# Kernel optimization log

Measured on AMD Instinct MI355X. Metric: run time of the kernel, lower is better.

Reference implementation:

```python
import jax, jax.numpy as jnp
import numpy as np

KSIZE = 51  # radius=50 is even -> incremented to 51 in __init__


def _gaussian_1d(ksize):
    # cv2.getGaussianKernel with sigma<=0: sigma = 0.3*((ksize-1)*0.5 - 1) + 0.8
    sigma = 0.3 * ((ksize - 1) * 0.5 - 1) + 0.8
    x = np.arange(ksize, dtype=np.float64) - (ksize - 1) / 2
    g = np.exp(-(x * x) / (2.0 * sigma * sigma))
    g = g / g.sum()
    return g.astype(np.float32)


def _blur(img, kernel1d):
    """Separable Gaussian blur with reflect padding.
    Mathematically identical to the 2D conv with outer(g, g) in the torch code.
    img: (b, c, h, w), kernel1d: (k,)
    """
    k = kernel1d.shape[0]
    p = k // 2
    b, c, h, w = img.shape
    x = jnp.pad(img, ((0, 0), (0, 0), (p, p), (p, p)), mode='reflect')
    x = x.reshape(b * c, 1, h + 2 * p, w + 2 * p)
    # vertical pass then horizontal pass (conv vs correlation irrelevant: symmetric kernel)
    kv = kernel1d.reshape(1, 1, k, 1)
    kh = kernel1d.reshape(1, 1, 1, k)
    dn = ('NCHW', 'OIHW', 'NCHW')
    x = jax.lax.conv_general_dilated(x, kv, (1, 1), 'VALID', dimension_numbers=dn)
    x = jax.lax.conv_general_dilated(x, kh, (1, 1), 'VALID', dimension_numbers=dn)
    return x.reshape(b, c, h, w)


def setup_inputs() -> dict:
    key = jax.random.key(0)
    img = jax.random.uniform(key, (16, 3, 512, 512), dtype=jnp.float32)
    kernel1d = jnp.asarray(_gaussian_1d(KSIZE))
    return {"img": img, "kernel1d": kernel1d}


def reference(img, kernel1d):
    weight = 0.5
    threshold = 10.0
    blur = _blur(img, kernel1d)
    residual = img - blur
    mask = (jnp.abs(residual) * 255.0 > threshold).astype(img.dtype)
    soft_mask = _blur(mask, kernel1d)
    sharp = jnp.clip(img + weight * residual, 0.0, 1.0)
    return soft_mask * sharp + (1.0 - soft_mask) * img
```

## Files before the change

### kernel.cpp

```cpp
#include <hip/hip_runtime.h>
#include <hip/hip_bf16.h>


constexpr int IMG = 512;
constexpr int NIMG = 48;
constexpr int K = 51, P = 25;
constexpr int CB = 64;
constexpr int RB = 128;
constexpr int WAVES = 8;
constexpr int VB = 16;
constexpr int NLOOP = VB + K - 1;
constexpr int TR = RB + 2 * P;
constexpr int TRS = RB + 1;
constexpr int LDS_FLOATS = TR * CB;

__device__ __forceinline__ float bf2f(unsigned short u) {
    unsigned int x = (unsigned int)u << 16;
    return __builtin_bit_cast(float, x);
}
__device__ __forceinline__ unsigned short f2bf(float f) {
    unsigned int u = __builtin_bit_cast(unsigned int, f);
    u += 0x7FFF + ((u >> 16) & 1);
    return (unsigned short)(u >> 16);
}

template <int SRCB, int LOADM, int STOREM>
__global__ __launch_bounds__(512) void pass_kern(const void* __restrict__ srcv,
                                                 const float* __restrict__ img,
                                                 const unsigned short* __restrict__ res,
                                                 void* __restrict__ dstv,
                                                 const float* __restrict__ k1d) {
    __shared__ float lds[LDS_FLOATS];
    const int lane = threadIdx.x & 63;
    const int wvu = __builtin_amdgcn_readfirstlane(threadIdx.x >> 6);
    const int c0 = blockIdx.x * CB;
    const int r0 = blockIdx.y * RB;
    const size_t base = (size_t)blockIdx.z * (IMG * IMG);

    for (int r = wvu; r < TR; r += WAVES) {
        int y = r0 - P + r;
        const int ya = y < 0 ? -y : y;
        y = min(ya, 2 * IMG - 2 - y);
        const size_t si = base + (size_t)y * IMG + c0 + lane;
        float v = SRCB ? bf2f(((const unsigned short*)srcv)[si])
                       : ((const float*)srcv)[si];
        if (LOADM == 1) v = (fabsf(v) * 255.0f > 10.0f) ? 1.0f : 0.0f;
        lds[r * CB + lane] = v;
    }

    float kern[K];
#pragma unroll
    for (int k = 0; k < K; ++k) kern[k] = k1d[k];

    __syncthreads();

    float acc[VB];
#pragma unroll
    for (int o = 0; o < VB; ++o) acc[o] = 0.f;

    const int trow0 = wvu * VB;
#pragma unroll
    for (int r = 0; r < NLOOP; ++r) {
        const float v = lds[(trow0 + r) * CB + lane];
#pragma unroll
        for (int o = 0; o < VB; ++o) {
            const int k = r - o;
            if (0 <= k && k < K) acc[o] = fmaf(kern[k], v, acc[o]);
        }
    }

    __syncthreads();

#pragma unroll
    for (int o = 0; o < VB; ++o) lds[lane * TRS + trow0 + o] = acc[o];
    __syncthreads();

#pragma unroll
    for (int i = 0; i < 8; ++i) {
        const int cc = wvu * 8 + i;
#pragma unroll
        for (int j = 0; j < 2; ++j) {
            const int rr = j * 64 + lane;
            const float bv = lds[cc * TRS + rr];
            const size_t di = base + (size_t)(c0 + cc) * IMG + (r0 + rr);
            if (STOREM == 0) {
                ((unsigned short*)dstv)[di] = f2bf(bv);
            } else if (STOREM == 1) {
                ((unsigned short*)dstv)[di] = f2bf(img[di] - bv);
            } else {
                const float iv = img[di];
                const float rv = bf2f(res[di]);
                float sharp = fmaf(0.5f, rv, iv);
                sharp = fminf(fmaxf(sharp, 0.f), 1.f);
                ((float*)dstv)[di] = fmaf(bv, sharp - iv, iv);
            }
        }
    }
}

extern "C" void kernel_launch(void* const* d_in, const int* in_sizes, int n_in,
                              void* d_out, int out_size, void* d_ws, size_t ws_size,
                              hipStream_t stream) {
    (void)in_sizes; (void)n_in; (void)out_size; (void)ws_size;
    const float* img = (const float*)d_in[0];
    const float* k1d = (const float*)d_in[1];
    float* out = (float*)d_out;
    unsigned short* vb = (unsigned short*)d_ws;
    unsigned short* rs = (unsigned short*)d_ws + (size_t)NIMG * IMG * IMG;

    const dim3 grid(IMG / CB, IMG / RB, NIMG);

    pass_kern<0, 0, 0><<<grid, 512, 0, stream>>>(img, nullptr, nullptr, vb, k1d);
    pass_kern<1, 0, 1><<<grid, 512, 0, stream>>>(vb, img, nullptr, rs, k1d);
    pass_kern<1, 1, 0><<<grid, 512, 0, stream>>>(rs, nullptr, nullptr, vb, k1d);
    pass_kern<1, 0, 2><<<grid, 512, 0, stream>>>(vb, img, rs, out, k1d);
}
```

Baseline: 100.9 us.

## Stage column tiles in LDS as swizzled bf16 and read four rows per load

The LDS staging buffer now holds bf16 values in a column-major, XOR-swizzled layout, so each lane reads four consecutive rows with a single 8-byte LDS load instead of one float per row. This cuts the number of LDS read instructions in the vertical convolution loop and shrinks the staging footprint. In exchange, the first pass now rounds the fp32 input to bf16 before convolving, which adds precision loss. Bit extraction and conversion instructions are also added to the inner loop.

```diff
diff --git a/kernel.cpp b/kernel.cpp
--- a/kernel.cpp
+++ b/kernel.cpp
@@ -10,9 +10,11 @@
 constexpr int WAVES = 8;
 constexpr int VB = 16;
 constexpr int NLOOP = VB + K - 1;
+constexpr int NCHUNK = 17;
 constexpr int TR = RB + 2 * P;
+constexpr int SROW = 256;
 constexpr int TRS = RB + 1;
-constexpr int LDS_FLOATS = TR * CB;
+constexpr int LDS_BYTES = CB * TRS * 4;
 
 __device__ __forceinline__ float bf2f(unsigned short u) {
     unsigned int x = (unsigned int)u << 16;
@@ -24,13 +26,20 @@
     return (unsigned short)(u >> 16);
 }
 
+__device__ __forceinline__ int sidx(int c, int r) {
+    return c * SROW + (r ^ ((c & 15) << 2));
+}
+
 template <int SRCB, int LOADM, int STOREM>
 __global__ __launch_bounds__(512) void pass_kern(const void* __restrict__ srcv,
                                                  const float* __restrict__ img,
                                                  const unsigned short* __restrict__ res,
                                                  void* __restrict__ dstv,
                                                  const float* __restrict__ k1d) {
-    __shared__ float lds[LDS_FLOATS];
+    __shared__ unsigned char ldsraw[LDS_BYTES];
+    unsigned short* st = (unsigned short*)ldsraw;
+    float* tr = (float*)ldsraw;
+
     const int lane = threadIdx.x & 63;
     const int wvu = __builtin_amdgcn_readfirstlane(threadIdx.x >> 6);
     const int c0 = blockIdx.x * CB;
@@ -42,10 +51,17 @@
         const int ya = y < 0 ? -y : y;
         y = min(ya, 2 * IMG - 2 - y);
         const size_t si = base + (size_t)y * IMG + c0 + lane;
-        float v = SRCB ? bf2f(((const unsigned short*)srcv)[si])
-                       : ((const float*)srcv)[si];
-        if (LOADM == 1) v = (fabsf(v) * 255.0f > 10.0f) ? 1.0f : 0.0f;
-        lds[r * CB + lane] = v;
+        unsigned short u;
+        if (SRCB) {
+            u = ((const unsigned short*)srcv)[si];
+            if (LOADM == 1) {
+                const float v = bf2f(u);
+                u = (fabsf(v) * 255.0f > 10.0f) ? 0x3F80 : 0;
+            }
+        } else {
+            u = f2bf(((const float*)srcv)[si]);
+        }
+        st[sidx(lane, r)] = u;
     }
 
     float kern[K];
@@ -59,20 +75,35 @@
     for (int o = 0; o < VB; ++o) acc[o] = 0.f;
 
     const int trow0 = wvu * VB;
+    const int sbase = lane * SROW;
+    const int sx = (lane & 15) << 2;
 #pragma unroll
-    for (int r = 0; r < NLOOP; ++r) {
-        const float v = lds[(trow0 + r) * CB + lane];
+    for (int t = 0; t < NCHUNK; ++t) {
+        const int rb4 = trow0 + 4 * t;
+        const uint2 ch = *(const uint2*)(&st[sbase + (rb4 ^ sx)]);
 #pragma unroll
-        for (int o = 0; o < VB; ++o) {
-            const int k = r - o;
-            if (0 <= k && k < K) acc[o] = fmaf(kern[k], v, acc[o]);
+        for (int i = 0; i < 4; ++i) {
+            const int r = 4 * t + i;
+            if (r < NLOOP) {
+                const unsigned short uu =
+                    (i == 0) ? (unsigned short)ch.x :
+                    (i == 1) ? (unsigned short)(ch.x >> 16) :
+                    (i == 2) ? (unsigned short)ch.y :
+                               (unsigned short)(ch.y >> 16);
+                const float v = bf2f(uu);
+#pragma unroll
+                for (int o = 0; o < VB; ++o) {
+                    const int k = r - o;
+                    if (0 <= k && k < K) acc[o] = fmaf(kern[k], v, acc[o]);
+                }
+            }
         }
     }
 
     __syncthreads();
 
 #pragma unroll
-    for (int o = 0; o < VB; ++o) lds[lane * TRS + trow0 + o] = acc[o];
+    for (int o = 0; o < VB; ++o) tr[lane * TRS + trow0 + o] = acc[o];
     __syncthreads();
 
 #pragma unroll
@@ -81,7 +112,7 @@
 #pragma unroll
         for (int j = 0; j < 2; ++j) {
             const int rr = j * 64 + lane;
-            const float bv = lds[cc * TRS + rr];
+            const float bv = tr[cc * TRS + rr];
             const size_t di = base + (size_t)(c0 + cc) * IMG + (r0 + rr);
             if (STOREM == 0) {
                 ((unsigned short*)dstv)[di] = f2bf(bv);
```

Result: slower. 107.5 us (+6.5%).

## Compute separable blur passes with bf16 MFMA against a banded Toeplitz weight matrix

Applied to the files above, without the earlier changes.

Each pass now builds a banded Toeplitz bf16 weight matrix in LDS and computes the 51-tap vertical convolution with 16x16x32 bf16 MFMA instructions, replacing scalar FMA loops. The input tile is stored in LDS as bf16 in a transposed, XOR-swizzled layout to avoid bank conflicts, and the LDS transpose staging before stores is removed, with outputs written as vectorized 4-element chunks. This cuts ALU work and LDS traffic. In exchange it rounds the input and kernel weights to bf16 (including the fp32 image in the first pass), which reduces accuracy.

```diff
diff --git a/kernel.cpp b/kernel.cpp
--- a/kernel.cpp
+++ b/kernel.cpp
@@ -2,98 +2,123 @@
 #include <hip/hip_bf16.h>
 
 
-constexpr int IMG = 512;
-constexpr int NIMG = 48;
-constexpr int K = 51, P = 25;
+typedef __attribute__((ext_vector_type(8))) short bf16x8;
+typedef __attribute__((ext_vector_type(4))) float f32x4;
+
+constexpr int IMG = 512, NIMG = 48, K = 51, P = 25;
 constexpr int CB = 64;
 constexpr int RB = 128;
 constexpr int WAVES = 8;
-constexpr int VB = 16;
-constexpr int NLOOP = VB + K - 1;
 constexpr int TR = RB + 2 * P;
-constexpr int TRS = RB + 1;
-constexpr int LDS_FLOATS = TR * CB;
+constexpr int SCH = 26;
+constexpr int SROW = 256;
+constexpr int NK = 96;
 
 __device__ __forceinline__ float bf2f(unsigned short u) {
-    unsigned int x = (unsigned int)u << 16;
-    return __builtin_bit_cast(float, x);
+    return __builtin_bit_cast(float, (unsigned)u << 16);
 }
 __device__ __forceinline__ unsigned short f2bf(float f) {
-    unsigned int u = __builtin_bit_cast(unsigned int, f);
+    unsigned u = __builtin_bit_cast(unsigned, f);
     u += 0x7FFF + ((u >> 16) & 1);
     return (unsigned short)(u >> 16);
 }
+__device__ __forceinline__ int sidx(int c, int s) {
+    return c * SROW + (s ^ ((c & 7) << 3));
+}
 
 template <int SRCB, int LOADM, int STOREM>
-__global__ __launch_bounds__(512) void pass_kern(const void* __restrict__ srcv,
-                                                 const float* __restrict__ img,
-                                                 const unsigned short* __restrict__ res,
-                                                 void* __restrict__ dstv,
-                                                 const float* __restrict__ k1d) {
-    __shared__ float lds[LDS_FLOATS];
-    const int lane = threadIdx.x & 63;
-    const int wvu = __builtin_amdgcn_readfirstlane(threadIdx.x >> 6);
+__global__ __launch_bounds__(512, 8) void pass_kern(const void* __restrict__ srcv,
+                                                    const float* __restrict__ img,
+                                                    const unsigned short* __restrict__ res,
+                                                    void* __restrict__ dstv,
+                                                    const float* __restrict__ k1d) {
+    __shared__ unsigned short st[CB * SROW];
+    __shared__ unsigned short wb[16 * NK];
+    const int tid = threadIdx.x, lane = tid & 63;
+    const int wv = __builtin_amdgcn_readfirstlane(tid >> 6);
     const int c0 = blockIdx.x * CB;
     const int r0 = blockIdx.y * RB;
     const size_t base = (size_t)blockIdx.z * (IMG * IMG);
 
-    for (int r = wvu; r < TR; r += WAVES) {
-        int y = r0 - P + r;
-        const int ya = y < 0 ? -y : y;
-        y = min(ya, 2 * IMG - 2 - y);
-        const size_t si = base + (size_t)y * IMG + c0 + lane;
-        float v = SRCB ? bf2f(((const unsigned short*)srcv)[si])
-                       : ((const float*)srcv)[si];
-        if (LOADM == 1) v = (fabsf(v) * 255.0f > 10.0f) ? 1.0f : 0.0f;
-        lds[r * CB + lane] = v;
+#pragma unroll
+    for (int e = 0; e < 3; ++e) {
+        const int idx = tid + e * 512;
+        const int i = idx / NK, r = idx - i * NK;
+        const int t = r - i;
+        wb[idx] = (t >= 0 && t < K) ? f2bf(k1d[t]) : (unsigned short)0;
     }
 
-    float kern[K];
+    for (int ch = wv; ch < SCH; ch += WAVES) {
+        const int s0 = ch * 8;
+        unsigned pk[4];
 #pragma unroll
-    for (int k = 0; k < K; ++k) kern[k] = k1d[k];
-
+        for (int j2 = 0; j2 < 4; ++j2) {
+            unsigned short uu[2];
+#pragma unroll
+            for (int h = 0; h < 2; ++h) {
+                const int s = s0 + j2 * 2 + h;
+                unsigned short u = 0;
+                if (s < TR) {
+                    int y = r0 - P + s;
+                    const int ya = y < 0 ? -y : y;
+                    y = min(ya, 2 * IMG - 2 - y);
+                    const size_t si = base + (size_t)y * IMG + c0 + lane;
+                    if (SRCB) {
+                        u = ((const unsigned short*)srcv)[si];
+                        if (LOADM == 1) u = (fabsf(bf2f(u)) * 255.0f > 10.0f) ? 0x3F80 : 0;
+                    } else {
+                        u = f2bf(((const float*)srcv)[si]);
+                    }
+                }
+                uu[h] = u;
+            }
+            pk[j2] = (unsigned)uu[0] | ((unsigned)uu[1] << 16);
+        }
+        *(uint4*)&st[sidx(lane, s0)] = make_uint4(pk[0], pk[1], pk[2], pk[3]);
+    }
     __syncthreads();
 
-    float acc[VB];
+    const int m = lane & 15, g = lane >> 4;
+    bf16x8 afr[3];
 #pragma unroll
-    for (int o = 0; o < VB; ++o) acc[o] = 0.f;
+    for (int rs = 0; rs < 3; ++rs)
+        afr[rs] = *(const bf16x8*)&wb[m * NK + rs * 32 + g * 8];
 
-    const int trow0 = wvu * VB;
+    const int y0 = wv * 16;
 #pragma unroll
-    for (int r = 0; r < NLOOP; ++r) {
-        const float v = lds[(trow0 + r) * CB + lane];
+    for (int ct = 0; ct < 4; ++ct) {
+        const int c = ct * 16 + m;
+        f32x4 acc = {0.f, 0.f, 0.f, 0.f};
 #pragma unroll
-        for (int o = 0; o < VB; ++o) {
-            const int k = r - o;
-            if (0 <= k && k < K) acc[o] = fmaf(kern[k], v, acc[o]);
+        for (int rs = 0; rs < 3; ++rs) {
+            const bf16x8 bfr = *(const bf16x8*)&st[sidx(c, y0 + rs * 32 + g * 8)];
+            acc = __builtin_amdgcn_mfma_f32_16x16x32_bf16(afr[rs], bfr, acc, 0, 0, 0);
         }
-    }
-
-    __syncthreads();
-
+        const int Cg = c0 + c;
+        const int Rg = r0 + y0 + g * 4;
+        const size_t di = base + (size_t)Cg * IMG + Rg;
+        if (STOREM == 0) {
+            const unsigned d0 = (unsigned)f2bf(acc[0]) | ((unsigned)f2bf(acc[1]) << 16);
+            const unsigned d1 = (unsigned)f2bf(acc[2]) | ((unsigned)f2bf(acc[3]) << 16);
+            *(uint2*)&((unsigned short*)dstv)[di] = make_uint2(d0, d1);
+        } else if (STOREM == 1) {
+            const f32x4 iv = *(const f32x4*)&img[di];
+            const unsigned d0 = (unsigned)f2bf(iv[0] - acc[0]) | ((unsigned)f2bf(iv[1] - acc[1]) << 16);
+            const unsigned d1 = (unsigned)f2bf(iv[2] - acc[2]) | ((unsigned)f2bf(iv[3] - acc[3]) << 16);
+            *(uint2*)&((unsigned short*)dstv)[di] = make_uint2(d0, d1);
+        } else {
+            const f32x4 iv = *(const f32x4*)&img[di];
+            const uint2 rv2 = *(const uint2*)&res[di];
+            f32x4 o;
 #pragma unroll
-    for (int o = 0; o < VB; ++o) lds[lane * TRS + trow0 + o] = acc[o];
-    __syncthreads();
-
-#pragma unroll
-    for (int i = 0; i < 8; ++i) {
-        const int cc = wvu * 8 + i;
-#pragma unroll
-        for (int j = 0; j < 2; ++j) {
-            const int rr = j * 64 + lane;
-            const float bv = lds[cc * TRS + rr];
-            const size_t di = base + (size_t)(c0 + cc) * IMG + (r0 + rr);
-            if (STOREM == 0) {
-                ((unsigned short*)dstv)[di] = f2bf(bv);
-            } else if (STOREM == 1) {
-                ((unsigned short*)dstv)[di] = f2bf(img[di] - bv);
-            } else {
-                const float iv = img[di];
-                const float rv = bf2f(res[di]);
-                float sharp = fmaf(0.5f, rv, iv);
+            for (int q = 0; q < 4; ++q) {
+                const unsigned rw = (q < 2) ? rv2.x : rv2.y;
+                const float rvq = bf2f((unsigned short)(rw >> ((q & 1) * 16)));
+                float sharp = fmaf(0.5f, rvq, iv[q]);
                 sharp = fminf(fmaxf(sharp, 0.f), 1.f);
-                ((float*)dstv)[di] = fmaf(bv, sharp - iv, iv);
+                o[q] = fmaf(acc[q], sharp - iv[q], iv[q]);
             }
+            *(f32x4*)&((float*)dstv)[di] = o;
         }
     }
 }
```

New measurement: 102.5 us. No clear change (+1.6%).

## Compute 1D blur passes as banded-matrix MFMA in bf16, reading rows directly

Applied to the files above, without the earlier changes.

Replaces the scalar FMA vertical-convolution pass with a banded Toeplitz matrix multiply on MFMA bf16 units. Each wave loads contiguous row segments straight from global memory as bf16x8 fragments, with no LDS staging of the input tile, and stores the result transposed. This is meant to move the 51-tap convolution arithmetic onto matrix cores and cut LDS traffic. The cost is converting the input and kernel weights to bf16, some wasted work in the zero-padded band (96 taps for 51), and strided transposed stores.

```diff
diff --git a/kernel.cpp b/kernel.cpp
--- a/kernel.cpp
+++ b/kernel.cpp
@@ -2,87 +2,102 @@
 #include <hip/hip_bf16.h>
 
 
-constexpr int IMG = 512;
-constexpr int NIMG = 48;
-constexpr int K = 51, P = 25;
-constexpr int CB = 64;
-constexpr int RB = 128;
-constexpr int WAVES = 8;
-constexpr int VB = 16;
-constexpr int NLOOP = VB + K - 1;
-constexpr int TR = RB + 2 * P;
-constexpr int TRS = RB + 1;
-constexpr int LDS_FLOATS = TR * CB;
+typedef __attribute__((ext_vector_type(8))) short bf16x8;
+typedef __attribute__((ext_vector_type(4))) float f32x4;
+
+constexpr int IMG = 512, NIMG = 48, K = 51;
 
 __device__ __forceinline__ float bf2f(unsigned short u) {
-    unsigned int x = (unsigned int)u << 16;
-    return __builtin_bit_cast(float, x);
+    return __builtin_bit_cast(float, (unsigned)u << 16);
 }
 __device__ __forceinline__ unsigned short f2bf(float f) {
-    unsigned int u = __builtin_bit_cast(unsigned int, f);
+    unsigned u = __builtin_bit_cast(unsigned, f);
     u += 0x7FFF + ((u >> 16) & 1);
     return (unsigned short)(u >> 16);
 }
+__device__ __forceinline__ int refl(int i) {
+    i = i < 0 ? -i : i;
+    return i >= IMG ? 2 * IMG - 2 - i : i;
+}
 
 template <int SRCB, int LOADM, int STOREM>
-__global__ __launch_bounds__(512) void pass_kern(const void* __restrict__ srcv,
-                                                 const float* __restrict__ img,
-                                                 const unsigned short* __restrict__ res,
-                                                 void* __restrict__ dstv,
-                                                 const float* __restrict__ k1d) {
-    __shared__ float lds[LDS_FLOATS];
-    const int lane = threadIdx.x & 63;
-    const int wvu = __builtin_amdgcn_readfirstlane(threadIdx.x >> 6);
-    const int c0 = blockIdx.x * CB;
-    const int r0 = blockIdx.y * RB;
-    const size_t base = (size_t)blockIdx.z * (IMG * IMG);
+__global__ __launch_bounds__(256) void xblur_kern(const void* __restrict__ srcv,
+                                                  const float* __restrict__ img,
+                                                  const unsigned short* __restrict__ res,
+                                                  void* __restrict__ dstv,
+                                                  const float* __restrict__ k1d) {
+    __shared__ unsigned short wb[16 * 96];
+    const int tid = threadIdx.x, lane = tid & 63;
+    const int wv = __builtin_amdgcn_readfirstlane(tid >> 6);
+    const int m16 = lane & 15, g = lane >> 4;
 
-    for (int r = wvu; r < TR; r += WAVES) {
-        int y = r0 - P + r;
-        const int ya = y < 0 ? -y : y;
-        y = min(ya, 2 * IMG - 2 - y);
-        const size_t si = base + (size_t)y * IMG + c0 + lane;
-        float v = SRCB ? bf2f(((const unsigned short*)srcv)[si])
-                       : ((const float*)srcv)[si];
-        if (LOADM == 1) v = (fabsf(v) * 255.0f > 10.0f) ? 1.0f : 0.0f;
-        lds[r * CB + lane] = v;
+#pragma unroll
+    for (int e = 0; e < 6; ++e) {
+        const int idx = tid + e * 256;
+        const int mm = idx / 96, kk = idx - mm * 96;
+        const int t = kk - mm - 7;
+        wb[idx] = (t >= 0 && t < K) ? f2bf(k1d[t]) : (unsigned short)0;
     }
-
-    float kern[K];
-#pragma unroll
-    for (int k = 0; k < K; ++k) kern[k] = k1d[k];
-
     __syncthreads();
 
-    float acc[VB];
+    bf16x8 a[3];
 #pragma unroll
-    for (int o = 0; o < VB; ++o) acc[o] = 0.f;
+    for (int rs = 0; rs < 3; ++rs)
+        a[rs] = *(const bf16x8*)&wb[m16 * 96 + rs * 32 + g * 8];
 
-    const int trow0 = wvu * VB;
+    const int u0 = blockIdx.x * 64;
+    const int v0 = (blockIdx.y * 4 + wv) * 16;
+    const size_t base = (size_t)blockIdx.z * (IMG * IMG);
+    const bool edge = (v0 < 32) || (v0 > 448);
+
+    f32x4 acc[4] = {{0.f, 0.f, 0.f, 0.f}, {0.f, 0.f, 0.f, 0.f},
+                    {0.f, 0.f, 0.f, 0.f}, {0.f, 0.f, 0.f, 0.f}};
+
 #pragma unroll
-    for (int r = 0; r < NLOOP; ++r) {
-        const float v = lds[(trow0 + r) * CB + lane];
+    for (int ut = 0; ut < 4; ++ut) {
+        const size_t urow = base + (size_t)(u0 + ut * 16 + m16) * IMG;
 #pragma unroll
-        for (int o = 0; o < VB; ++o) {
-            const int k = r - o;
-            if (0 <= k && k < K) acc[o] = fmaf(kern[k], v, acc[o]);
+        for (int rs = 0; rs < 3; ++rs) {
+            const int vk = v0 - 32 + rs * 32 + g * 8;
+            bf16x8 b;
+            if (!edge) {
+                if (SRCB) {
+                    b = *(const bf16x8*)&((const unsigned short*)srcv)[urow + vk];
+                } else {
+                    const f32x4 f0 = *(const f32x4*)&((const float*)srcv)[urow + vk];
+                    const f32x4 f1 = *(const f32x4*)&((const float*)srcv)[urow + vk + 4];
+#pragma unroll
+                    for (int j = 0; j < 4; ++j) {
+                        b[j] = (short)f2bf(f0[j]);
+                        b[j + 4] = (short)f2bf(f1[j]);
+                    }
+                }
+            } else {
+#pragma unroll
+                for (int j = 0; j < 8; ++j) {
+                    const int vv = refl(vk + j);
+                    b[j] = SRCB ? (short)((const unsigned short*)srcv)[urow + vv]
+                                : (short)f2bf(((const float*)srcv)[urow + vv]);
+                }
+            }
+            if (LOADM == 1) {
+#pragma unroll
+                for (int j = 0; j < 8; ++j) {
+                    const unsigned short uu = (unsigned short)b[j];
+                    b[j] = (short)(((uu & 0x7FFFu) > 0x3D20u) ? 0x3F80 : 0);
+                }
+            }
+            acc[ut] = __builtin_amdgcn_mfma_f32_16x16x32_bf16(a[rs], b, acc[ut], 0, 0, 0);
         }
     }
 
-    __syncthreads();
-
 #pragma unroll
-    for (int o = 0; o < VB; ++o) lds[lane * TRS + trow0 + o] = acc[o];
-    __syncthreads();
-
+    for (int ut = 0; ut < 4; ++ut) {
+        const int u = u0 + ut * 16 + m16;
 #pragma unroll
-    for (int i = 0; i < 8; ++i) {
-        const int cc = wvu * 8 + i;
-#pragma unroll
-        for (int j = 0; j < 2; ++j) {
-            const int rr = j * 64 + lane;
-            const float bv = lds[cc * TRS + rr];
-            const size_t di = base + (size_t)(c0 + cc) * IMG + (r0 + rr);
+        for (int q = 0; q < 4; ++q) {
+            const size_t di = base + (size_t)(v0 + 4 * g + q) * IMG + u;
+            const float bv = acc[ut][q];
             if (STOREM == 0) {
                 ((unsigned short*)dstv)[di] = f2bf(bv);
             } else if (STOREM == 1) {
@@ -105,13 +120,13 @@
     const float* img = (const float*)d_in[0];
     const float* k1d = (const float*)d_in[1];
     float* out = (float*)d_out;
-    unsigned short* vb = (unsigned short*)d_ws;
+    unsigned short* t1 = (unsigned short*)d_ws;
     unsigned short* rs = (unsigned short*)d_ws + (size_t)NIMG * IMG * IMG;
 
-    const dim3 grid(IMG / CB, IMG / RB, NIMG);
+    const dim3 grid(IMG / 64, IMG / 64, NIMG);
 
-    pass_kern<0, 0, 0><<<grid, 512, 0, stream>>>(img, nullptr, nullptr, vb, k1d);
-    pass_kern<1, 0, 1><<<grid, 512, 0, stream>>>(vb, img, nullptr, rs, k1d);
-    pass_kern<1, 1, 0><<<grid, 512, 0, stream>>>(rs, nullptr, nullptr, vb, k1d);
-    pass_kern<1, 0, 2><<<grid, 512, 0, stream>>>(vb, img, rs, out, k1d);
+    xblur_kern<0, 0, 0><<<grid, 256, 0, stream>>>(img, nullptr, nullptr, t1, k1d);
+    xblur_kern<1, 0, 1><<<grid, 256, 0, stream>>>(t1, img, nullptr, rs, k1d);
+    xblur_kern<1, 1, 0><<<grid, 256, 0, stream>>>(rs, nullptr, nullptr, t1, k1d);
+    xblur_kern<1, 0, 2><<<grid, 256, 0, stream>>>(t1, img, rs, out, k1d);
 }
```

After: 336.5 us. 3.33x slower.
